# Performance work log

Measured on AMD Instinct MI355X. Metric: run time of the kernel, lower is better.

## Reference

```python
import jax, jax.numpy as jnp
import numpy as np

EPS = 1e-5


def _two_qubit_block(xa, xb, pa, pb, ga, gb):
    """Analytic 2-qubit state-vector sim (real amplitudes, Ry/CNOT only).
    Circuit: Ry(xa)q0, Ry(xb)q1, Ry(pa)q0, Ry(pb)q1, CNOT(0,1), Ry(ga)q0, Ry(gb)q1.
    Returns (<Z0>, <Z1>) batched over xa/xb shape."""
    ha = 0.5 * (xa + pa)  # consecutive Ry angles add
    hb = 0.5 * (xb + pb)
    ca, sa = jnp.cos(ha), jnp.sin(ha)
    cb, sb = jnp.cos(hb), jnp.sin(hb)
    # product state amplitudes psi[i,j]
    p00, p01, p10, p11 = ca * cb, ca * sb, sa * cb, sa * sb
    # CNOT(control=0, target=1): swap |10> <-> |11>
    p10, p11 = p11, p10
    # Ry(ga) on qubit 0
    cg, sg = jnp.cos(0.5 * ga), jnp.sin(0.5 * ga)
    q00 = cg * p00 - sg * p10
    q10 = sg * p00 + cg * p10
    q01 = cg * p01 - sg * p11
    q11 = sg * p01 + cg * p11
    # Ry(gb) on qubit 1
    ch, sh = jnp.cos(0.5 * gb), jnp.sin(0.5 * gb)
    r00 = ch * q00 - sh * q01
    r01 = sh * q00 + ch * q01
    r10 = ch * q10 - sh * q11
    r11 = sh * q10 + ch * q11
    z0 = r00 ** 2 + r01 ** 2 - r10 ** 2 - r11 ** 2
    z1 = r00 ** 2 - r01 ** 2 + r10 ** 2 - r11 ** 2
    return z0, z1


def _forward(x, qparams, in_proj_w, in_proj_b, out_proj_w, out_proj_b,
             ln_w, ln_b, lin_w, lin_b):
    B = x.shape[0]
    xi = x.reshape(B, 28, 28)
    # extract 2x2 patches in order [x[r,c], x[r,c+1], x[r+1,c], x[r+1,c+1]]
    patches = xi.reshape(B, 14, 2, 14, 2).transpose(0, 1, 3, 2, 4).reshape(B, 196, 4)
    # vectorized quantum kernel: qubits (0,1) and (2,3) are independent 2-qubit blocks
    z0, z1 = _two_qubit_block(patches[..., 0], patches[..., 1],
                              qparams[0], qparams[1], qparams[4], qparams[5])
    z2, z3 = _two_qubit_block(patches[..., 2], patches[..., 3],
                              qparams[2], qparams[3], qparams[6], qparams[7])
    seq = jnp.stack([z0, z1, z2, z3], axis=-1)  # (B, 196, 4)

    # MultiheadAttention: embed_dim=4, heads=2, head_dim=2 (eval mode, no dropout)
    E, H, D, L = 4, 2, 2, 196
    qkv = seq @ in_proj_w.T + in_proj_b  # (B, L, 12)
    q, k, v = jnp.split(qkv, 3, axis=-1)
    q = q.reshape(B, L, H, D)
    k = k.reshape(B, L, H, D)
    v = v.reshape(B, L, H, D)
    scores = jnp.einsum('blhd,bmhd->bhlm', q, k) / jnp.sqrt(jnp.asarray(D, q.dtype))
    attn = jax.nn.softmax(scores, axis=-1)
    o = jnp.einsum('bhlm,bmhd->blhd', attn, v).reshape(B, L, E)
    o = o @ out_proj_w.T + out_proj_b  # (B, L, 4)

    # LayerNorm over the channel dim (size 4)
    mu = o.mean(axis=-1, keepdims=True)
    var = o.var(axis=-1, keepdims=True)
    o = (o - mu) / jnp.sqrt(var + EPS) * ln_w + ln_b

    # permute to (B, 4, 196) then flatten to match linear's 4*14*14 layout
    flat = o.transpose(0, 2, 1).reshape(B, 4 * 196)
    logits = flat @ lin_w.T + lin_b
    return jax.nn.log_softmax(logits, axis=-1)


def setup_inputs() -> dict:
    key = jax.random.key(0)
    ks = jax.random.split(key, 8)
    B, E, L = 2048, 4, 196
    x = jax.random.uniform(ks[0], (B, 1, 28, 28), dtype=jnp.float32)
    qparams = jax.random.normal(ks[1], (8,), dtype=jnp.float32)
    in_proj_w = jax.random.normal(ks[2], (3 * E, E), dtype=jnp.float32) * (1.0 / np.sqrt(E))
    in_proj_b = jnp.zeros((3 * E,), dtype=jnp.float32)
    out_proj_w = jax.random.normal(ks[3], (E, E), dtype=jnp.float32) * (1.0 / np.sqrt(E))
    out_proj_b = jnp.zeros((E,), dtype=jnp.float32)
    ln_w = jnp.ones((E,), dtype=jnp.float32)
    ln_b = jnp.zeros((E,), dtype=jnp.float32)
    lin_w = jax.random.normal(ks[4], (10, E * L), dtype=jnp.float32) * (1.0 / np.sqrt(E * L))
    lin_b = jnp.zeros((10,), dtype=jnp.float32)
    return {"x": x, "qparams": qparams, "in_proj_w": in_proj_w, "in_proj_b": in_proj_b,
            "out_proj_w": out_proj_w, "out_proj_b": out_proj_b,
            "ln_w": ln_w, "ln_b": ln_b, "lin_w": lin_w, "lin_b": lin_b}


def reference(x, qparams, in_proj_w, in_proj_b, out_proj_w, out_proj_b,
              ln_w, ln_b, lin_w, lin_b):
    return _forward(x, qparams, in_proj_w, in_proj_b, out_proj_w, out_proj_b,
                    ln_w, ln_b, lin_w, lin_b)
```

## Files before the change

### kernel.cpp

```cpp
#include <hip/hip_runtime.h>
#include <hip/hip_bf16.h>

#define NTHREADS 256
#define EPSF 1e-5f
#define QSCALE 1.0201606003163899f

typedef float v2f __attribute__((ext_vector_type(2)));
typedef float v4f __attribute__((ext_vector_type(4)));

#if __has_builtin(__builtin_amdgcn_exp2f)
#define EXP2F(x) __builtin_amdgcn_exp2f(x)
#else
extern "C" __device__ float __ocml_native_exp2_f32(float);
#define EXP2F(x) __ocml_native_exp2_f32(x)
#endif

__device__ __forceinline__ void two_qubit(float xa, float xb, float pa, float pb,
                                          float cg, float sg, float ch, float sh,
                                          float& z0, float& z1) {
    const float ha = 0.5f * (xa + pa);
    const float hb = 0.5f * (xb + pb);
    float sa, ca, sb, cb;
    __sincosf(ha, &sa, &ca);
    __sincosf(hb, &sb, &cb);
    const float p00 = ca * cb, p01 = ca * sb;
    const float p10 = sa * sb, p11 = sa * cb;
    const float q00 = cg * p00 - sg * p10;
    const float q10 = sg * p00 + cg * p10;
    const float q01 = cg * p01 - sg * p11;
    const float q11 = sg * p01 + cg * p11;
    const float r00 = ch * q00 - sh * q01;
    const float r01 = sh * q00 + ch * q01;
    const float r10 = ch * q10 - sh * q11;
    const float r11 = sh * q10 + ch * q11;
    const float a = r00 * r00, b = r01 * r01, c = r10 * r10, d = r11 * r11;
    z0 = a + b - c - d;
    z1 = a - b + c - d;
}

__global__ __launch_bounds__(NTHREADS)
void quanv_fused(const float* __restrict__ x,
                 const float* __restrict__ qparams,
                 const float* __restrict__ in_w,
                 const float* __restrict__ in_b,
                 const float* __restrict__ out_w,
                 const float* __restrict__ out_b,
                 const float* __restrict__ lnw,
                 const float* __restrict__ lnb,
                 const float* __restrict__ lin_w,
                 const float* __restrict__ lin_b,
                 float* __restrict__ out)
{
    __shared__ __align__(16) float img_flat[784];
    __shared__ __align__(8)  float2 qs[2][196];
    __shared__ v4f kT[2][98];
    __shared__ v4f vT[2][98];
    __shared__ __align__(16) float ob[196][4];
    __shared__ float w_in[48], b_in[12], w_out[16], b_out[4];
    __shared__ float s_lnw[4], s_lnb[4], s_linb[10];
    __shared__ float qc[8];
    __shared__ float qp[4];
    __shared__ float wsum[4][10];
    __shared__ float logits_s[10];
    __shared__ float lse_s;

    const int tid = threadIdx.x;
    const int bid = blockIdx.x;

    const float4* xb4 = (const float4*)(x + (size_t)bid * 784);
    if (tid < 196) ((float4*)img_flat)[tid] = xb4[tid];
    if (tid < 48) w_in[tid] = in_w[tid];
    {
        int t = tid - 64;  if (t >= 0 && t < 12) b_in[t] = in_b[t];
        t = tid - 80;      if (t >= 0 && t < 16) w_out[t] = out_w[t];
        t = tid - 96;      if (t >= 0 && t < 4)  b_out[t] = out_b[t];
        t = tid - 112;     if (t >= 0 && t < 4)  s_lnw[t] = lnw[t];
        t = tid - 128;     if (t >= 0 && t < 4)  s_lnb[t] = lnb[t];
        t = tid - 144;     if (t >= 0 && t < 10) s_linb[t] = lin_b[t];
        t = tid - 160;     if (t >= 0 && t < 4)  qp[t] = qparams[t];
        t = tid - 176;
        if (t >= 0 && t < 4) {
            const float g = 0.5f * qparams[4 + t];
            float sg, cg;
            __sincosf(g, &sg, &cg);
            qc[2 * t] = cg;
            qc[2 * t + 1] = sg;
        }
    }
    __syncthreads();

    if (tid < 196) {
        const int l = tid;
        const int r = l / 14, c = l % 14;
        const float p0 = img_flat[(2 * r) * 28 + 2 * c];
        const float p1 = img_flat[(2 * r) * 28 + 2 * c + 1];
        const float p2 = img_flat[(2 * r + 1) * 28 + 2 * c];
        const float p3 = img_flat[(2 * r + 1) * 28 + 2 * c + 1];
        float z0, z1, z2, z3;
        two_qubit(p0, p1, qp[0], qp[1], qc[0], qc[1], qc[2], qc[3], z0, z1);
        two_qubit(p2, p3, qp[2], qp[3], qc[4], qc[5], qc[6], qc[7], z2, z3);
        float a[12];
        #pragma unroll
        for (int j = 0; j < 12; ++j)
            a[j] = b_in[j] + z0 * w_in[j * 4] + z1 * w_in[j * 4 + 1]
                 + z2 * w_in[j * 4 + 2] + z3 * w_in[j * 4 + 3];
        qs[0][l] = make_float2(a[0] * QSCALE, a[1] * QSCALE);
        qs[1][l] = make_float2(a[2] * QSCALE, a[3] * QSCALE);
        const int i4 = l >> 1, e = l & 1;
        ((float*)&kT[0][i4])[e]     = a[4];
        ((float*)&kT[0][i4])[2 + e] = a[5];
        ((float*)&kT[1][i4])[e]     = a[6];
        ((float*)&kT[1][i4])[2 + e] = a[7];
        ((float*)&vT[0][i4])[e]     = a[8];
        ((float*)&vT[0][i4])[2 + e] = a[9];
        ((float*)&vT[1][i4])[e]     = a[10];
        ((float*)&vT[1][i4])[2 + e] = a[11];
    }
    __syncthreads();

    const int wv = tid >> 6;
    const int lane = tid & 63;
    const int h = wv >> 1;
    const int lbase = (wv & 1) * 98;
    const int halfsel = lane >> 5;
    const int sub = lane & 31;
    const v4f* kTp = &kT[h][0];
    const v4f* vTp = &vT[h][0];
    #pragma unroll
    for (int p = 0; p < 3; ++p) {
        const int l = lbase + p * 32 + sub;
        const float2 q = qs[h][l];
        const int i0 = halfsel * 49;
        v2f sum2 = {0.f, 0.f}, acc0 = {0.f, 0.f}, acc1 = {0.f, 0.f};
        #pragma unroll 7
        for (int i = 0; i < 49; ++i) {
            const v4f kk = kTp[i0 + i];
            const v4f vv = vTp[i0 + i];
            const v2f s = kk.xy * q.x + kk.zw * q.y;
            v2f e;
            e.x = EXP2F(s.x);
            e.y = EXP2F(s.y);
            sum2 += e;
            acc0 += e * vv.xy;
            acc1 += e * vv.zw;
        }
        float sum = sum2.x + sum2.y;
        float a0  = acc0.x + acc0.y;
        float a1  = acc1.x + acc1.y;
        sum += __shfl_xor(sum, 32);
        a0  += __shfl_xor(a0, 32);
        a1  += __shfl_xor(a1, 32);
        if (halfsel == 0) {
            const float inv = 1.0f / sum;
            *(float2*)&ob[l][2 * h] = make_float2(a0 * inv, a1 * inv);
        }
    }
    {
        const int grp = lane >> 4;
        const int sub16 = lane & 15;
        const int l = lbase + 96 + (grp >> 1);
        const int hs = grp & 1;
        const float2 q = qs[h][l];
        const int base = hs * 49;
        v2f sum2 = {0.f, 0.f}, acc0 = {0.f, 0.f}, acc1 = {0.f, 0.f};
        #pragma unroll
        for (int k = 0; k < 3; ++k) {
            const int i = base + sub16 + k * 16;
            const v4f kk = kTp[i];
            const v4f vv = vTp[i];
            const v2f s = kk.xy * q.x + kk.zw * q.y;
            v2f e;
            e.x = EXP2F(s.x);
            e.y = EXP2F(s.y);
            sum2 += e;
            acc0 += e * vv.xy;
            acc1 += e * vv.zw;
        }
        if (sub16 == 0) {
            const int i = base + 48;
            const v4f kk = kTp[i];
            const v4f vv = vTp[i];
            const v2f s = kk.xy * q.x + kk.zw * q.y;
            v2f e;
            e.x = EXP2F(s.x);
            e.y = EXP2F(s.y);
            sum2 += e;
            acc0 += e * vv.xy;
            acc1 += e * vv.zw;
        }
        float sum = sum2.x + sum2.y;
        float a0  = acc0.x + acc0.y;
        float a1  = acc1.x + acc1.y;
        #pragma unroll
        for (int off = 1; off < 32; off <<= 1) {
            sum += __shfl_xor(sum, off);
            a0  += __shfl_xor(a0, off);
            a1  += __shfl_xor(a1, off);
        }
        if ((lane & 31) == 0) {
            const float inv = 1.0f / sum;
            *(float2*)&ob[l][2 * h] = make_float2(a0 * inv, a1 * inv);
        }
    }
    __syncthreads();

    if (tid < 196) {
        const int l = tid;
        const float4 f = *(const float4*)ob[l];
        const float f0 = f.x, f1 = f.y, f2 = f.z, f3 = f.w;
        const float e0 = b_out[0] + f0 * w_out[0]  + f1 * w_out[1]  + f2 * w_out[2]  + f3 * w_out[3];
        const float e1 = b_out[1] + f0 * w_out[4]  + f1 * w_out[5]  + f2 * w_out[6]  + f3 * w_out[7];
        const float e2 = b_out[2] + f0 * w_out[8]  + f1 * w_out[9]  + f2 * w_out[10] + f3 * w_out[11];
        const float e3 = b_out[3] + f0 * w_out[12] + f1 * w_out[13] + f2 * w_out[14] + f3 * w_out[15];
        const float mu = 0.25f * (e0 + e1 + e2 + e3);
        const float d0 = e0 - mu, d1 = e1 - mu, d2 = e2 - mu, d3 = e3 - mu;
        const float var = 0.25f * (d0 * d0 + d1 * d1 + d2 * d2 + d3 * d3);
        const float rs = rsqrtf(var + EPSF);
        img_flat[0 * 196 + l] = d0 * rs * s_lnw[0] + s_lnb[0];
        img_flat[1 * 196 + l] = d1 * rs * s_lnw[1] + s_lnb[1];
        img_flat[2 * 196 + l] = d2 * rs * s_lnw[2] + s_lnb[2];
        img_flat[3 * 196 + l] = d3 * rs * s_lnw[3] + s_lnb[3];
    }
    __syncthreads();

    float part[10];
    #pragma unroll
    for (int j = 0; j < 10; ++j) part[j] = 0.f;
    if (tid < 196) {
        const float4 f = ((const float4*)img_flat)[tid];
        const float4* lw = (const float4*)lin_w + tid;
        #pragma unroll
        for (int j = 0; j < 10; ++j) {
            const float4 w = lw[j * 196];
            part[j] = f.x * w.x + f.y * w.y + f.z * w.z + f.w * w.w;
        }
    }
    const int wlane = tid & 63, wvv = tid >> 6;
    #pragma unroll
    for (int j = 0; j < 10; ++j) {
        float v = part[j];
        #pragma unroll
        for (int off = 32; off > 0; off >>= 1) v += __shfl_down(v, off);
        if (wlane == 0) wsum[wvv][j] = v;
    }
    __syncthreads();
    if (tid < 10)
        logits_s[tid] = wsum[0][tid] + wsum[1][tid] + wsum[2][tid]
                      + wsum[3][tid] + s_linb[tid];
    __syncthreads();
    if (tid == 0) {
        float mx = logits_s[0];
        #pragma unroll
        for (int j = 1; j < 10; ++j) mx = fmaxf(mx, logits_s[j]);
        float se = 0.f;
        #pragma unroll
        for (int j = 0; j < 10; ++j) se += __expf(logits_s[j] - mx);
        lse_s = mx + __logf(se);
    }
    __syncthreads();
    if (tid < 10) out[(size_t)bid * 10 + tid] = logits_s[tid] - lse_s;
}

extern "C" void kernel_launch(void* const* d_in, const int* in_sizes, int n_in,
                              void* d_out, int out_size, void* d_ws, size_t ws_size,
                              hipStream_t stream) {
    const float* x        = (const float*)d_in[0];
    const float* qparams  = (const float*)d_in[1];
    const float* in_w     = (const float*)d_in[2];
    const float* in_b     = (const float*)d_in[3];
    const float* out_w    = (const float*)d_in[4];
    const float* out_b    = (const float*)d_in[5];
    const float* lnw      = (const float*)d_in[6];
    const float* lnb      = (const float*)d_in[7];
    const float* lin_w    = (const float*)d_in[8];
    const float* lin_b    = (const float*)d_in[9];
    float* out            = (float*)d_out;

    const int B = in_sizes[0] / 784;
    hipLaunchKernelGGL(quanv_fused, dim3(B), dim3(NTHREADS), 0, stream,
                       x, qparams, in_w, in_b, out_w, out_b, lnw, lnb, lin_w, lin_b, out);
}
```

Baseline: 41.51 us.

## Split attention keys across waves and register-block three queries per lane

Reassigns the attention work so each wave owns one head and one half of the keys, with every lane holding three queries and reusing each loaded K/V vector across all three. Partial softmax sums and accumulators go to shared memory (aliased onto the image buffer), and a later combine step merges the two key halves and normalises. This cuts LDS loads per exp and removes the cross-half shuffle. In exchange it adds an extra barrier, extra shared-memory traffic and more live registers.

```diff
diff --git a/kernel.cpp b/kernel.cpp
--- a/kernel.cpp
+++ b/kernel.cpp
@@ -51,11 +51,10 @@
                  const float* __restrict__ lin_b,
                  float* __restrict__ out)
 {
-    __shared__ __align__(16) float img_flat[784];
+    __shared__ __align__(16) float uni[2352];
     __shared__ __align__(8)  float2 qs[2][196];
     __shared__ v4f kT[2][98];
     __shared__ v4f vT[2][98];
-    __shared__ __align__(16) float ob[196][4];
     __shared__ float w_in[48], b_in[12], w_out[16], b_out[4];
     __shared__ float s_lnw[4], s_lnb[4], s_linb[10];
     __shared__ float qc[8];
@@ -64,11 +63,15 @@
     __shared__ float logits_s[10];
     __shared__ float lse_s;
 
+    float* psum = uni;
+    float* pa0  = uni + 784;
+    float* pa1  = uni + 1568;
+
     const int tid = threadIdx.x;
     const int bid = blockIdx.x;
 
     const float4* xb4 = (const float4*)(x + (size_t)bid * 784);
-    if (tid < 196) ((float4*)img_flat)[tid] = xb4[tid];
+    if (tid < 196) ((float4*)uni)[tid] = xb4[tid];
     if (tid < 48) w_in[tid] = in_w[tid];
     {
         int t = tid - 64;  if (t >= 0 && t < 12) b_in[t] = in_b[t];
@@ -92,10 +95,10 @@
     if (tid < 196) {
         const int l = tid;
         const int r = l / 14, c = l % 14;
-        const float p0 = img_flat[(2 * r) * 28 + 2 * c];
-        const float p1 = img_flat[(2 * r) * 28 + 2 * c + 1];
-        const float p2 = img_flat[(2 * r + 1) * 28 + 2 * c];
-        const float p3 = img_flat[(2 * r + 1) * 28 + 2 * c + 1];
+        const float p0 = uni[(2 * r) * 28 + 2 * c];
+        const float p1 = uni[(2 * r) * 28 + 2 * c + 1];
+        const float p2 = uni[(2 * r + 1) * 28 + 2 * c];
+        const float p3 = uni[(2 * r + 1) * 28 + 2 * c + 1];
         float z0, z1, z2, z3;
         two_qubit(p0, p1, qp[0], qp[1], qc[0], qc[1], qc[2], qc[3], z0, z1);
         two_qubit(p2, p3, qp[2], qp[3], qc[4], qc[5], qc[6], qc[7], z2, z3);
@@ -121,51 +124,54 @@
     const int wv = tid >> 6;
     const int lane = tid & 63;
     const int h = wv >> 1;
-    const int lbase = (wv & 1) * 98;
-    const int halfsel = lane >> 5;
-    const int sub = lane & 31;
-    const v4f* kTp = &kT[h][0];
-    const v4f* vTp = &vT[h][0];
-    #pragma unroll
-    for (int p = 0; p < 3; ++p) {
-        const int l = lbase + p * 32 + sub;
-        const float2 q = qs[h][l];
-        const int i0 = halfsel * 49;
-        v2f sum2 = {0.f, 0.f}, acc0 = {0.f, 0.f}, acc1 = {0.f, 0.f};
+    const int hs = wv & 1;
+    const int i0 = hs * 49;
+    const int pbase = h * 392 + hs * 196;
+    {
+        float2 q[3];
+        v2f sum2[3], ac0[3], ac1[3];
+        #pragma unroll
+        for (int r = 0; r < 3; ++r) {
+            q[r] = qs[h][lane + r * 64];
+            sum2[r] = (v2f){0.f, 0.f};
+            ac0[r]  = (v2f){0.f, 0.f};
+            ac1[r]  = (v2f){0.f, 0.f};
+        }
+        const v4f* kTp = &kT[h][i0];
+        const v4f* vTp = &vT[h][i0];
         #pragma unroll 7
         for (int i = 0; i < 49; ++i) {
-            const v4f kk = kTp[i0 + i];
-            const v4f vv = vTp[i0 + i];
-            const v2f s = kk.xy * q.x + kk.zw * q.y;
-            v2f e;
-            e.x = EXP2F(s.x);
-            e.y = EXP2F(s.y);
-            sum2 += e;
-            acc0 += e * vv.xy;
-            acc1 += e * vv.zw;
-        }
-        float sum = sum2.x + sum2.y;
-        float a0  = acc0.x + acc0.y;
-        float a1  = acc1.x + acc1.y;
-        sum += __shfl_xor(sum, 32);
-        a0  += __shfl_xor(a0, 32);
-        a1  += __shfl_xor(a1, 32);
-        if (halfsel == 0) {
-            const float inv = 1.0f / sum;
-            *(float2*)&ob[l][2 * h] = make_float2(a0 * inv, a1 * inv);
+            const v4f kk = kTp[i];
+            const v4f vv = vTp[i];
+            #pragma unroll
+            for (int r = 0; r < 3; ++r) {
+                const v2f s = kk.xy * q[r].x + kk.zw * q[r].y;
+                v2f e;
+                e.x = EXP2F(s.x);
+                e.y = EXP2F(s.y);
+                sum2[r] += e;
+                ac0[r]  += e * vv.xy;
+                ac1[r]  += e * vv.zw;
+            }
+        }
+        #pragma unroll
+        for (int r = 0; r < 3; ++r) {
+            const int l = lane + r * 64;
+            psum[pbase + l] = sum2[r].x + sum2[r].y;
+            pa0[pbase + l]  = ac0[r].x + ac0[r].y;
+            pa1[pbase + l]  = ac1[r].x + ac1[r].y;
         }
     }
     {
-        const int grp = lane >> 4;
-        const int sub16 = lane & 15;
-        const int l = lbase + 96 + (grp >> 1);
-        const int hs = grp & 1;
+        const int g = lane >> 4, s16 = lane & 15;
+        const int l = 192 + g;
         const float2 q = qs[h][l];
-        const int base = hs * 49;
-        v2f sum2 = {0.f, 0.f}, acc0 = {0.f, 0.f}, acc1 = {0.f, 0.f};
+        const v4f* kTp = &kT[h][0];
+        const v4f* vTp = &vT[h][0];
+        v2f sum2 = {0.f, 0.f}, ac0 = {0.f, 0.f}, ac1 = {0.f, 0.f};
         #pragma unroll
         for (int k = 0; k < 3; ++k) {
-            const int i = base + sub16 + k * 16;
+            const int i = i0 + s16 + k * 16;
             const v4f kk = kTp[i];
             const v4f vv = vTp[i];
             const v2f s = kk.xy * q.x + kk.zw * q.y;
@@ -173,41 +179,51 @@
             e.x = EXP2F(s.x);
             e.y = EXP2F(s.y);
             sum2 += e;
-            acc0 += e * vv.xy;
-            acc1 += e * vv.zw;
-        }
-        if (sub16 == 0) {
-            const int i = base + 48;
-            const v4f kk = kTp[i];
-            const v4f vv = vTp[i];
+            ac0 += e * vv.xy;
+            ac1 += e * vv.zw;
+        }
+        if (s16 == 0) {
+            const v4f kk = kTp[i0 + 48];
+            const v4f vv = vTp[i0 + 48];
             const v2f s = kk.xy * q.x + kk.zw * q.y;
             v2f e;
             e.x = EXP2F(s.x);
             e.y = EXP2F(s.y);
             sum2 += e;
-            acc0 += e * vv.xy;
-            acc1 += e * vv.zw;
+            ac0 += e * vv.xy;
+            ac1 += e * vv.zw;
         }
         float sum = sum2.x + sum2.y;
-        float a0  = acc0.x + acc0.y;
-        float a1  = acc1.x + acc1.y;
-        #pragma unroll
-        for (int off = 1; off < 32; off <<= 1) {
+        float a0  = ac0.x + ac0.y;
+        float a1  = ac1.x + ac1.y;
+        #pragma unroll
+        for (int off = 1; off < 16; off <<= 1) {
             sum += __shfl_xor(sum, off);
             a0  += __shfl_xor(a0, off);
             a1  += __shfl_xor(a1, off);
         }
-        if ((lane & 31) == 0) {
-            const float inv = 1.0f / sum;
-            *(float2*)&ob[l][2 * h] = make_float2(a0 * inv, a1 * inv);
-        }
-    }
-    __syncthreads();
-
+        if (s16 == 0) {
+            psum[pbase + l] = sum;
+            pa0[pbase + l]  = a0;
+            pa1[pbase + l]  = a1;
+        }
+    }
+    __syncthreads();
+
+    float f0, f1, f2, f3;
     if (tid < 196) {
         const int l = tid;
-        const float4 f = *(const float4*)ob[l];
-        const float f0 = f.x, f1 = f.y, f2 = f.z, f3 = f.w;
+        const float s0 = psum[l]       + psum[196 + l];
+        const float s1 = psum[392 + l] + psum[588 + l];
+        const float i0h = 1.0f / s0, i1h = 1.0f / s1;
+        f0 = (pa0[l]       + pa0[196 + l]) * i0h;
+        f1 = (pa1[l]       + pa1[196 + l]) * i0h;
+        f2 = (pa0[392 + l] + pa0[588 + l]) * i1h;
+        f3 = (pa1[392 + l] + pa1[588 + l]) * i1h;
+    }
+    __syncthreads();
+    if (tid < 196) {
+        const int l = tid;
         const float e0 = b_out[0] + f0 * w_out[0]  + f1 * w_out[1]  + f2 * w_out[2]  + f3 * w_out[3];
         const float e1 = b_out[1] + f0 * w_out[4]  + f1 * w_out[5]  + f2 * w_out[6]  + f3 * w_out[7];
         const float e2 = b_out[2] + f0 * w_out[8]  + f1 * w_out[9]  + f2 * w_out[10] + f3 * w_out[11];
@@ -216,10 +232,10 @@
         const float d0 = e0 - mu, d1 = e1 - mu, d2 = e2 - mu, d3 = e3 - mu;
         const float var = 0.25f * (d0 * d0 + d1 * d1 + d2 * d2 + d3 * d3);
         const float rs = rsqrtf(var + EPSF);
-        img_flat[0 * 196 + l] = d0 * rs * s_lnw[0] + s_lnb[0];
-        img_flat[1 * 196 + l] = d1 * rs * s_lnw[1] + s_lnb[1];
-        img_flat[2 * 196 + l] = d2 * rs * s_lnw[2] + s_lnb[2];
-        img_flat[3 * 196 + l] = d3 * rs * s_lnw[3] + s_lnb[3];
+        uni[0 * 196 + l] = d0 * rs * s_lnw[0] + s_lnb[0];
+        uni[1 * 196 + l] = d1 * rs * s_lnw[1] + s_lnb[1];
+        uni[2 * 196 + l] = d2 * rs * s_lnw[2] + s_lnb[2];
+        uni[3 * 196 + l] = d3 * rs * s_lnw[3] + s_lnb[3];
     }
     __syncthreads();
 
@@ -227,7 +243,7 @@
     #pragma unroll
     for (int j = 0; j < 10; ++j) part[j] = 0.f;
     if (tid < 196) {
-        const float4 f = ((const float4*)img_flat)[tid];
+        const float4 f = ((const float4*)uni)[tid];
         const float4* lw = (const float4*)lin_w + tid;
         #pragma unroll
         for (int j = 0; j < 10; ++j) {
@@ -235,13 +251,12 @@
             part[j] = f.x * w.x + f.y * w.y + f.z * w.z + f.w * w.w;
         }
     }
-    const int wlane = tid & 63, wvv = tid >> 6;
     #pragma unroll
     for (int j = 0; j < 10; ++j) {
         float v = part[j];
         #pragma unroll
         for (int off = 32; off > 0; off >>= 1) v += __shfl_down(v, off);
-        if (wlane == 0) wsum[wvv][j] = v;
+        if (lane == 0) wsum[wv][j] = v;
     }
     __syncthreads();
     if (tid < 10)
```

New measurement: 37.02 us, median of 2. 1.12x faster.
